# Kernel tuning notes

Measured on AMD Instinct MI355X. Metric: run time of the kernel, lower is better.

The kernel has to match this reference:

```python
import jax, jax.numpy as jnp
import numpy as np

FEATURE_DIM = 512


def setup_inputs() -> dict:
    key = jax.random.key(0)
    ks = jax.random.split(key, 12)
    B, Nv, Dv = 32, 1024, 768
    Nl, Dl = 77, 512
    D = FEATURE_DIM
    s = lambda fan_in: 1.0 / np.sqrt(fan_in)
    return {
        "fv": jax.random.normal(ks[0], (B, Nv, Dv), jnp.float32),
        "fl": jax.random.normal(ks[1], (B, Nl, Dl), jnp.float32),
        # linear_vk / linear_vv: Dv -> D (stored as [in, out])
        "W_vk": jax.random.uniform(ks[2], (Dv, D), jnp.float32, -s(Dv), s(Dv)),
        "b_vk": jax.random.uniform(ks[3], (D,), jnp.float32, -s(Dv), s(Dv)),
        "W_vv": jax.random.uniform(ks[4], (Dv, D), jnp.float32, -s(Dv), s(Dv)),
        "b_vv": jax.random.uniform(ks[5], (D,), jnp.float32, -s(Dv), s(Dv)),
        # linear_lk / linear_lv: Dl -> D
        "W_lk": jax.random.uniform(ks[6], (Dl, D), jnp.float32, -s(Dl), s(Dl)),
        "b_lk": jax.random.uniform(ks[7], (D,), jnp.float32, -s(Dl), s(Dl)),
        "W_lv": jax.random.uniform(ks[8], (Dl, D), jnp.float32, -s(Dl), s(Dl)),
        "b_lv": jax.random.uniform(ks[9], (D,), jnp.float32, -s(Dl), s(Dl)),
        # linear_m: nl(77) -> 768
        "W_m": jax.random.uniform(ks[10], (Nl, 768), jnp.float32, -s(Nl), s(Nl)),
        "b_m": jax.random.uniform(ks[11], (768,), jnp.float32, -s(Nl), s(Nl)),
    }


def reference(fv, fl, W_vk, b_vk, W_vv, b_vv, W_lk, b_lk, W_lv, b_lv, W_m, b_m):
    # projections
    fk_v = jnp.einsum("bvd,de->bve", fv, W_vk) + b_vk   # [B, Nv, D]
    fv_v = jnp.einsum("bvd,de->bve", fv, W_vv) + b_vv   # [B, Nv, D]
    fk_l = jnp.einsum("bld,de->ble", fl, W_lk) + b_lk   # [B, Nl, D]
    fv_l = jnp.einsum("bld,de->ble", fl, W_lv) + b_lv   # [B, Nl, D]
    # shared score matrix [B, Nl, Nv]
    a_raw = jnp.einsum("ble,bve->blv", fk_l, fk_v) / jnp.sqrt(
        jnp.asarray(FEATURE_DIM, fk_l.dtype))
    # dual softmax: over Nv for language queries, over Nl for vision queries
    fa_v = jnp.einsum("blv,bve->ble", jax.nn.softmax(a_raw, axis=-1), fv_v)  # [B, Nl, D]
    fa_l = jnp.einsum("bvl,ble->bve",
                      jax.nn.softmax(jnp.swapaxes(a_raw, -1, -2), axis=-1),
                      fv_l)                                                  # [B, Nv, D]
    # fm = fa_v @ fa_l^T -> [B, Nl, Nv]; transpose(1,2) -> [B, Nv, Nl]
    fm = jnp.einsum("bve,ble->bvl", fa_l, fa_v)          # [B, Nv, Nl]
    return jnp.einsum("bvl,lo->bvo", fm, W_m) + b_m      # [B, Nv, 768]
```

## Files before the change

### kernel.cpp

```cpp
#include <hip/hip_runtime.h>


using s16x8  = __attribute__((ext_vector_type(8))) short;
using f32x4v = __attribute__((ext_vector_type(4))) float;

__device__ __forceinline__ unsigned short f2bf(float f) {
  unsigned int u = __float_as_uint(f);
  u += 0x7fffu + ((u >> 16) & 1u);
  return (unsigned short)(u >> 16);
}
__device__ __forceinline__ float bf2f(unsigned short h) {
  return __uint_as_float(((unsigned int)h) << 16);
}
__device__ __forceinline__ void split2(float v, unsigned short &hh, unsigned short &ll) {
  hh = f2bf(v);
  ll = f2bf(v - bf2f(hh));
}
__device__ __forceinline__ void split8v(float4 a, float4 b, s16x8& H, s16x8& L) {
  unsigned short hh, ll;
  split2(a.x, hh, ll); H[0] = (short)hh; L[0] = (short)ll;
  split2(a.y, hh, ll); H[1] = (short)hh; L[1] = (short)ll;
  split2(a.z, hh, ll); H[2] = (short)hh; L[2] = (short)ll;
  split2(a.w, hh, ll); H[3] = (short)hh; L[3] = (short)ll;
  split2(b.x, hh, ll); H[4] = (short)hh; L[4] = (short)ll;
  split2(b.y, hh, ll); H[5] = (short)hh; L[5] = (short)ll;
  split2(b.z, hh, ll); H[6] = (short)hh; L[6] = (short)ll;
  split2(b.w, hh, ll); H[7] = (short)hh; L[7] = (short)ll;
}

__device__ __forceinline__ void gload16(const unsigned short* g, unsigned short* l) {
  __builtin_amdgcn_global_load_lds(
      (const __attribute__((address_space(1))) unsigned int*)(const void*)g,
      (__attribute__((address_space(3))) unsigned int*)(void*)l,
      16, 0, 0);
}

__global__ __launch_bounds__(256) void prep_weight(const float* __restrict__ W,
                                                   unsigned short* __restrict__ Wh,
                                                   unsigned short* __restrict__ Wl,
                                                   int K, int N, int Kpad) {
  __shared__ float tile[32][33];
  int nb = blockIdx.x * 32, kb = blockIdx.y * 32;
  int tx = threadIdx.x & 31, ty = threadIdx.x >> 5;
  #pragma unroll
  for (int i = 0; i < 32; i += 8) {
    int k = kb + ty + i, n = nb + tx;
    tile[ty + i][tx] = (k < K && n < N) ? W[(long)k * N + n] : 0.f;
  }
  __syncthreads();
  #pragma unroll
  for (int i = 0; i < 32; i += 8) {
    int n = nb + ty + i, k = kb + tx;
    if (n < N && k < Kpad) {
      unsigned short hh, ll;
      split2(tile[tx][ty + i], hh, ll);
      Wh[(long)n * Kpad + k] = hh;
      Wl[(long)n * Kpad + k] = ll;
    }
  }
}

struct GemmArgs {
  const unsigned short *Ah, *Alo, *Bh, *Blo;
  const float *Af;
  int K;
  int Mld, Nld;
  int lda, ldb;
  long long sA, sB;
};

template <bool AF32, bool SWZ, class Epi>
__global__ __launch_bounds__(256, 2) void gemm2(GemmArgs g, Epi epi) {
  __shared__ __align__(16) unsigned short sm[32768];

  int bidx = blockIdx.x, bidy = blockIdx.y;
  if constexpr (SWZ) {
    int nx = gridDim.x;
    int nwg = nx * gridDim.y;
    int orig = bidx + bidy * nx;
    int swz = (orig & 7) * (nwg >> 3) + (orig >> 3);
    bidx = swz % nx; bidy = swz / nx;
  }

  const int t    = threadIdx.x;
  const int b    = blockIdx.z;
  const int m0   = bidy * 128;
  const int n0   = bidx * 128;
  const int lane = t & 63;
  const int w    = t >> 6;
  const int wr   = (w >> 1) * 64;
  const int wc   = (w & 1) * 64;

  const long long aBase = (long long)b * g.sA;
  const long long bBase = (long long)b * g.sB;

  const int rw  = (w << 5) + (lane >> 2);
  const int cl  = lane & 3;
  const int sck = ((cl ^ ((rw >> 1) & 3)) << 3);
  int br0 = n0 + rw;      if (br0 > g.Nld - 1) br0 = g.Nld - 1;
  int br1 = n0 + rw + 16; if (br1 > g.Nld - 1) br1 = g.Nld - 1;
  const long long bR0d = bBase + (long long)br0 * g.ldb + sck;
  const long long bR1d = bBase + (long long)br1 * g.ldb + sck;
  int ar0 = m0 + rw;      if (ar0 > g.Mld - 1) ar0 = g.Mld - 1;
  int ar1 = m0 + rw + 16; if (ar1 > g.Mld - 1) ar1 = g.Mld - 1;
  const long long aR0d = aBase + (long long)ar0 * g.lda + sck;
  const long long aR1d = aBase + (long long)ar1 * g.lda + sck;
  const int dQ0 = w * 1024;
  const int dQ1 = w * 1024 + 512;

  const int rA0 = t >> 2, rA1 = 64 + (t >> 2), cc = t & 3;
  const int cOff = cc << 3;
  int mr0 = m0 + rA0; if (mr0 > g.Mld - 1) mr0 = g.Mld - 1;
  int mr1 = m0 + rA1; if (mr1 > g.Mld - 1) mr1 = g.Mld - 1;
  const long long aR0 = aBase + (long long)mr0 * g.lda;
  const long long aR1 = aBase + (long long)mr1 * g.lda;
  const int wA0 = rA0 * 32 + ((cc ^ ((rA0 >> 1) & 3)) << 3);
  const int wA1 = rA1 * 32 + ((cc ^ ((rA1 >> 1) & 3)) << 3);

  int roffA[4], roffB[4];
  #pragma unroll
  for (int i = 0; i < 4; ++i) {
    int row = wr + i * 16 + (lane & 15);
    int ch  = lane >> 4;
    roffA[i] = row * 32 + ((ch ^ ((row >> 1) & 3)) << 3);
    row = wc + i * 16 + (lane & 15);
    roffB[i] = row * 32 + ((ch ^ ((row >> 1) & 3)) << 3);
  }

  f32x4v acc[4][4];
  #pragma unroll
  for (int i = 0; i < 4; ++i)
    #pragma unroll
    for (int j = 0; j < 4; ++j)
      #pragma unroll
      for (int r = 0; r < 4; ++r) acc[i][j][r] = 0.f;

  float4 pa0, pa1, pa2, pa3;

  auto issueDMA = [&](int k0, int p) {
    unsigned short* bb = sm + p * 16384;
    gload16(g.Bh  + (bR0d + k0), bb + 8192  + dQ0);
    gload16(g.Bh  + (bR1d + k0), bb + 8192  + dQ1);
    gload16(g.Blo + (bR0d + k0), bb + 12288 + dQ0);
    gload16(g.Blo + (bR1d + k0), bb + 12288 + dQ1);
    if constexpr (!AF32) {
      gload16(g.Ah  + (aR0d + k0), bb + dQ0);
      gload16(g.Ah  + (aR1d + k0), bb + dQ1);
      gload16(g.Alo + (aR0d + k0), bb + 4096 + dQ0);
      gload16(g.Alo + (aR1d + k0), bb + 4096 + dQ1);
    }
  };
  auto issueLoadsA = [&](int k0) {
    if constexpr (AF32) {
      const float* s0 = g.Af + (aR0 + k0 + cOff);
      const float* s1 = g.Af + (aR1 + k0 + cOff);
      pa0 = *(const float4*)s0; pa1 = *(const float4*)(s0 + 4);
      pa2 = *(const float4*)s1; pa3 = *(const float4*)(s1 + 4);
    }
  };
  auto writeStageA = [&](int p) {
    if constexpr (AF32) {
      unsigned short* base = sm + p * 16384;
      s16x8 H, L;
      split8v(pa0, pa1, H, L);
      *(s16x8*)(base + wA0) = H; *(s16x8*)(base + 4096 + wA0) = L;
      split8v(pa2, pa3, H, L);
      *(s16x8*)(base + wA1) = H; *(s16x8*)(base + 4096 + wA1) = L;
    }
  };

  issueDMA(0, 0);
  issueLoadsA(0);
  writeStageA(0);
  int p = 0;
  const int nkt = g.K >> 5;
  for (int kt = 0; kt < nkt; ++kt) {
    asm volatile("s_waitcnt vmcnt(0)" ::: "memory");
    __syncthreads();
    if (kt + 1 < nkt) {
      issueDMA((kt + 1) << 5, p ^ 1);
      issueLoadsA((kt + 1) << 5);
    }
    unsigned short* base = sm + p * 16384;
    s16x8 ah[4], al[4], bh[4], bl[4];
    #pragma unroll
    for (int i = 0; i < 4; ++i) {
      ah[i] = *(const s16x8*)(base + roffA[i]);
      al[i] = *(const s16x8*)(base + 4096 + roffA[i]);
    }
    #pragma unroll
    for (int j = 0; j < 4; ++j) {
      bh[j] = *(const s16x8*)(base + 8192  + roffB[j]);
      bl[j] = *(const s16x8*)(base + 12288 + roffB[j]);
    }
    #pragma unroll
    for (int i = 0; i < 4; ++i)
      #pragma unroll
      for (int j = 0; j < 4; ++j) {
        acc[i][j] = __builtin_amdgcn_mfma_f32_16x16x32_bf16(ah[i], bh[j], acc[i][j], 0, 0, 0);
        acc[i][j] = __builtin_amdgcn_mfma_f32_16x16x32_bf16(ah[i], bl[j], acc[i][j], 0, 0, 0);
        acc[i][j] = __builtin_amdgcn_mfma_f32_16x16x32_bf16(al[i], bh[j], acc[i][j], 0, 0, 0);
      }
    if (kt + 1 < nkt) writeStageA(p ^ 1);
    p ^= 1;
  }
  #pragma unroll
  for (int i = 0; i < 4; ++i)
    #pragma unroll
    for (int j = 0; j < 4; ++j) {
      int mm = m0 + wr + i * 16 + ((lane >> 4) << 2);
      int nn = n0 + wc + j * 16 + (lane & 15);
      epi(b, mm, nn, acc[i][j]);
    }
}

struct EpiBF16Pair {
  unsigned short *h, *lo; const float* bias; long long bs; int ld; int Mst;
  __device__ void operator()(int b, int m, int n, f32x4v v) const {
    float bb = bias ? bias[n] : 0.f;
    #pragma unroll
    for (int r = 0; r < 4; ++r) {
      int mm = m + r;
      if (mm < Mst) {
        long long o = (long long)b * bs + (long long)mm * ld + n;
        unsigned short hh, ll;
        split2(v[r] + bb, hh, ll);
        h[o] = hh; lo[o] = ll;
      }
    }
  }
};

struct EpiDualL {
  unsigned short *kh, *kl, *vh, *vl; const float *bk, *bv;
  __device__ void operator()(int, int m, int n, f32x4v v) const {
    bool lo512 = n < 512;
    float bb = lo512 ? bk[n] : bv[n - 512];
    int nn = lo512 ? n : n - 512;
    unsigned short* H = lo512 ? kh : vh;
    unsigned short* L = lo512 ? kl : vl;
    #pragma unroll
    for (int r = 0; r < 4; ++r) {
      int mm = m + r;
      if (mm < 2464) {
        long long o = (long long)mm * 512 + nn;
        unsigned short hh, ll;
        split2(v[r] + bb, hh, ll);
        H[o] = hh; L[o] = ll;
      }
    }
  }
};

struct EpiDualV {
  unsigned short *kh, *kl, *vh, *vl; const float *bk, *bv;
  __device__ void operator()(int, int m, int n, f32x4v v) const {
    if (n < 512) {
      float bb = bk[n];
      #pragma unroll
      for (int r = 0; r < 4; ++r) {
        long long o = (long long)(m + r) * 512 + n;
        unsigned short hh, ll;
        split2(v[r] + bb, hh, ll);
        kh[o] = hh; kl[o] = ll;
      }
    } else {
      int b2 = m >> 10, vv = m & 1023;
      float bb = bv[n - 512];
      ushort4 H, L;
      split2(v[0] + bb, H.x, L.x); split2(v[1] + bb, H.y, L.y);
      split2(v[2] + bb, H.z, L.z); split2(v[3] + bb, H.w, L.w);
      long long o = ((long long)b2 * 512 + (n - 512)) * 1024 + vv;
      *(ushort4*)(vh + o) = H;
      *(ushort4*)(vl + o) = L;
    }
  }
};

struct EpiScore {
  float* out;
  __device__ void operator()(int b, int m, int n, f32x4v v) const {
    #pragma unroll
    for (int r = 0; r < 4; ++r) {
      int mm = m + r;
      if (mm < 77)
        out[((long long)b * 77 + mm) * 1024 + n] = v[r] * 0.04419417382415922f;
    }
  }
};

struct EpiTransT {
  unsigned short *h, *lo;
  __device__ void operator()(int b, int m, int n, f32x4v v) const {
    #pragma unroll
    for (int r = 0; r < 4; ++r) {
      int mm = m + r;
      float val = (mm < 77) ? v[r] : 0.f;
      long long o = (long long)b * 98304 + (long long)n * 128 + mm;
      unsigned short hh, ll;
      split2(val, hh, ll);
      h[o] = hh; lo[o] = ll;
    }
  }
};

struct EpiOutB {
  float* out; const float* bias;
  __device__ void operator()(int b, int m, int n, f32x4v v) const {
    float bb = bias[n];
    #pragma unroll
    for (int r = 0; r < 4; ++r)
      out[(long long)(b * 1024 + m + r) * 768 + n] = v[r] + bb;
  }
};

__global__ __launch_bounds__(256) void softmax_rows(const float* __restrict__ a,
                                                    unsigned short* __restrict__ Ph,
                                                    unsigned short* __restrict__ Plo) {
  long row = blockIdx.x;
  const float* src = a + row * 1024;
  int t = threadIdx.x;
  float4 x = ((const float4*)src)[t];
  float mx = fmaxf(fmaxf(x.x, x.y), fmaxf(x.z, x.w));
  #pragma unroll
  for (int o = 32; o; o >>= 1) mx = fmaxf(mx, __shfl_xor(mx, o));
  __shared__ float red[4], red2[4];
  int w = t >> 6;
  if ((t & 63) == 0) red[w] = mx;
  __syncthreads();
  mx = fmaxf(fmaxf(red[0], red[1]), fmaxf(red[2], red[3]));
  float e0 = __expf(x.x - mx), e1 = __expf(x.y - mx);
  float e2 = __expf(x.z - mx), e3 = __expf(x.w - mx);
  float s = e0 + e1 + e2 + e3;
  #pragma unroll
  for (int o = 32; o; o >>= 1) s += __shfl_xor(s, o);
  if ((t & 63) == 0) red2[w] = s;
  __syncthreads();
  s = red2[0] + red2[1] + red2[2] + red2[3];
  float inv = 1.f / s;
  ushort4 H, L;
  split2(e0 * inv, H.x, L.x); split2(e1 * inv, H.y, L.y);
  split2(e2 * inv, H.z, L.z); split2(e3 * inv, H.w, L.w);
  long o = row * 1024 + (long)t * 4;
  *(ushort4*)(Ph + o)  = H;
  *(ushort4*)(Plo + o) = L;
}

__global__ __launch_bounds__(128) void softmax_cols(const float* __restrict__ a,
                                                    unsigned short* __restrict__ Ph,
                                                    unsigned short* __restrict__ Plo) {
  __shared__ float tile[77 * 129];
  __shared__ float inv[128];
  int t = threadIdx.x;
  int c = blockIdx.x;
  int b = blockIdx.y;
  const float* src = a + (long)b * 77 * 1024 + c * 128;
  for (int r = 0; r < 77; ++r) tile[r * 129 + t] = src[(long)r * 1024 + t];
  __syncthreads();
  float mx = -1e30f;
  for (int r = 0; r < 77; ++r) mx = fmaxf(mx, tile[r * 129 + t]);
  float s = 0.f;
  for (int r = 0; r < 77; ++r) {
    float e = __expf(tile[r * 129 + t] - mx);
    tile[r * 129 + t] = e;
    s += e;
  }
  inv[t] = 1.f / s;
  __syncthreads();
  unsigned short* dh = Ph  + ((long)b * 1024 + c * 128) * 128;
  unsigned short* dl = Plo + ((long)b * 1024 + c * 128) * 128;
  for (int vb = 0; vb < 128; vb += 2) {
    int v = vb + (t >> 6);
    int k = (t & 63) * 2;
    float iv = inv[v];
    float p0 = (k     < 77) ? tile[k * 129 + v] * iv       : 0.f;
    float p1 = (k + 1 < 77) ? tile[(k + 1) * 129 + v] * iv : 0.f;
    ushort2 H, L;
    split2(p0, H.x, L.x); split2(p1, H.y, L.y);
    *(ushort2*)(dh + (long)v * 128 + k) = H;
    *(ushort2*)(dl + (long)v * 128 + k) = L;
  }
}

extern "C" void kernel_launch(void* const* d_in, const int* in_sizes, int n_in,
                              void* d_out, int out_size, void* d_ws, size_t ws_size,
                              hipStream_t stream) {
  const float* fv   = (const float*)d_in[0];
  const float* fl   = (const float*)d_in[1];
  const float* W_vk = (const float*)d_in[2];
  const float* b_vk = (const float*)d_in[3];
  const float* W_vv = (const float*)d_in[4];
  const float* b_vv = (const float*)d_in[5];
  const float* W_lk = (const float*)d_in[6];
  const float* b_lk = (const float*)d_in[7];
  const float* W_lv = (const float*)d_in[8];
  const float* b_lv = (const float*)d_in[9];
  const float* W_m  = (const float*)d_in[10];
  const float* b_m  = (const float*)d_in[11];

  char* base = (char*)d_ws;
  size_t off = 0;
  auto take = [&](size_t bytes) -> char* {
    char* p = base + off;
    off = (off + bytes + 255) & ~(size_t)255;
    return p;
  };

  unsigned short* wcatv_h = (unsigned short*)take(1572864);
  unsigned short* wcatv_l = (unsigned short*)take(1572864);
  unsigned short* wcatl_h = (unsigned short*)take(1048576);
  unsigned short* wcatl_l = (unsigned short*)take(1048576);
  unsigned short* wm_h    = (unsigned short*)take(196608);
  unsigned short* wm_l    = (unsigned short*)take(196608);
  unsigned short* fkl_h  = (unsigned short*)take(2523136);
  unsigned short* fkl_l  = (unsigned short*)take(2523136);
  unsigned short* fvl_h  = (unsigned short*)take(2523136);
  unsigned short* fvl_l  = (unsigned short*)take(2523136);
  unsigned short* fkv_h  = (unsigned short*)take(33554432);
  unsigned short* fkv_l  = (unsigned short*)take(33554432);
  unsigned short* fvvT_h = (unsigned short*)take(33554432);
  unsigned short* fvvT_l = (unsigned short*)take(33554432);
  float*          araw   = (float*)take(10092544);
  unsigned short* p1_h   = (unsigned short*)take(5046272);
  unsigned short* p1_l   = (unsigned short*)take(5046272);
  unsigned short* p2t_h  = (unsigned short*)take(8388608);
  unsigned short* p2t_l  = (unsigned short*)take(8388608);
  unsigned short* fav_h  = (unsigned short*)take(4194304);
  unsigned short* fav_l  = (unsigned short*)take(4194304);
  unsigned short* s_h    = (unsigned short*)take(1048576);
  unsigned short* s_l    = (unsigned short*)take(1048576);
  unsigned short* tt_h   = (unsigned short*)take(6291456);
  unsigned short* tt_l   = (unsigned short*)take(6291456);

  if (off > ws_size) return;

  prep_weight<<<dim3(16, 24), 256, 0, stream>>>(W_vk, wcatv_h, wcatv_l, 768, 512, 768);
  prep_weight<<<dim3(16, 24), 256, 0, stream>>>(W_vv, wcatv_h + 512 * 768, wcatv_l + 512 * 768, 768, 512, 768);
  prep_weight<<<dim3(16, 16), 256, 0, stream>>>(W_lk, wcatl_h, wcatl_l, 512, 512, 512);
  prep_weight<<<dim3(16, 16), 256, 0, stream>>>(W_lv, wcatl_h + 512 * 512, wcatl_l + 512 * 512, 512, 512, 512);
  prep_weight<<<dim3(24, 4), 256, 0, stream>>>(W_m, wm_h, wm_l, 77, 768, 128);

  {
    GemmArgs g{}; g.Af = fl; g.Bh = wcatl_h; g.Blo = wcatl_l;
    g.K = 512; g.Mld = 2464; g.Nld = 1024; g.lda = 512; g.ldb = 512; g.sA = 0; g.sB = 0;
    EpiDualL e{fkl_h, fkl_l, fvl_h, fvl_l, b_lk, b_lv};
    gemm2<true, false, EpiDualL><<<dim3(8, 20, 1), 256, 0, stream>>>(g, e);
  }
  {
    GemmArgs g{}; g.Af = fv; g.Bh = wcatv_h; g.Blo = wcatv_l;
    g.K = 768; g.Mld = 32768; g.Nld = 1024; g.lda = 768; g.ldb = 768; g.sA = 0; g.sB = 0;
    EpiDualV e{fkv_h, fkv_l, fvvT_h, fvvT_l, b_vk, b_vv};
    gemm2<true, true, EpiDualV><<<dim3(8, 256, 1), 256, 0, stream>>>(g, e);
  }
  {
    GemmArgs g{}; g.Ah = fkl_h; g.Alo = fkl_l; g.Bh = fkv_h; g.Blo = fkv_l;
    g.K = 512; g.Mld = 77; g.Nld = 1024; g.lda = 512; g.ldb = 512;
    g.sA = 77 * 512; g.sB = 1024 * 512;
    EpiScore e{araw};
    gemm2<false, false, EpiScore><<<dim3(8, 1, 32), 256, 0, stream>>>(g, e);
  }
  softmax_rows<<<2464, 256, 0, stream>>>(araw, p1_h, p1_l);
  softmax_cols<<<dim3(8, 32), 128, 0, stream>>>(araw, p2t_h, p2t_l);
  {
    GemmArgs g{}; g.Ah = p1_h; g.Alo = p1_l; g.Bh = fvvT_h; g.Blo = fvvT_l;
    g.K = 1024; g.Mld = 77; g.Nld = 512; g.lda = 1024; g.ldb = 1024;
    g.sA = 77 * 1024; g.sB = 512 * 1024;
    EpiBF16Pair e{fav_h, fav_l, nullptr, 128 * 512, 512, 128};
    gemm2<false, false, EpiBF16Pair><<<dim3(4, 1, 32), 256, 0, stream>>>(g, e);
  }
  {
    GemmArgs g{}; g.Ah = fvl_h; g.Alo = fvl_l; g.Bh = fav_h; g.Blo = fav_l;
    g.K = 512; g.Mld = 77; g.Nld = 128; g.lda = 512; g.ldb = 512;
    g.sA = 77 * 512; g.sB = 128 * 512;
    EpiBF16Pair e{s_h, s_l, nullptr, 128 * 128, 128, 128};
    gemm2<false, false, EpiBF16Pair><<<dim3(1, 1, 32), 256, 0, stream>>>(g, e);
  }
  {
    GemmArgs g{}; g.Ah = s_h; g.Alo = s_l; g.Bh = wm_h; g.Blo = wm_l;
    g.K = 128; g.Mld = 128; g.Nld = 768; g.lda = 128; g.ldb = 128;
    g.sA = 128 * 128; g.sB = 0;
    EpiTransT e{tt_h, tt_l};
    gemm2<false, false, EpiTransT><<<dim3(6, 1, 32), 256, 0, stream>>>(g, e);
  }
  {
    GemmArgs g{}; g.Ah = p2t_h; g.Alo = p2t_l; g.Bh = tt_h; g.Blo = tt_l;
    g.K = 128; g.Mld = 1024; g.Nld = 768; g.lda = 128; g.ldb = 128;
    g.sA = 1024 * 128; g.sB = 768 * 128;
    EpiOutB e{(float*)d_out, b_m};
    gemm2<false, false, EpiOutB><<<dim3(6, 8, 32), 256, 0, stream>>>(g, e);
  }
  (void)in_sizes; (void)n_in; (void)out_size;
}
```

Measured before the change: 585.7 us.

## Single-buffer GEMM LDS, raise occupancy, and add narrow-N tiles for small GEMMs

The GEMM kernel drops its LDS double buffer for a single stage with an extra barrier per k-step, and raises launch bounds from 2 to 4 blocks per CU. It is also templated on the N-tile width, so the small batched GEMMs use 64-wide N tiles and launch twice as many blocks. The aim is more resident waves to hide latency and better CU fill for the tiny per-batch GEMMs. The cost is that global loads are no longer overlapped with MFMA compute within a block, and the tighter register budget may cause spills.

```diff
diff --git a/kernel.cpp b/kernel.cpp
--- a/kernel.cpp
+++ b/kernel.cpp
@@ -69,9 +69,16 @@
   long long sA, sB;
 };
 
-template <bool AF32, bool SWZ, class Epi>
-__global__ __launch_bounds__(256, 2) void gemm2(GemmArgs g, Epi epi) {
-  __shared__ __align__(16) unsigned short sm[32768];
+template <bool AF32, bool SWZ, int NJ, class Epi>
+__global__ __launch_bounds__(256, 4) void gemm3(GemmArgs g, Epi epi) {
+  constexpr int BN  = NJ * 32;
+  constexpr int ASZ = 128 * 32;
+  constexpr int BSZ = BN * 32;
+  __shared__ __align__(16) unsigned short sm[2 * ASZ + 2 * BSZ];
+  unsigned short* sAh = sm;
+  unsigned short* sAl = sm + ASZ;
+  unsigned short* sBh = sm + 2 * ASZ;
+  unsigned short* sBl = sm + 2 * ASZ + BSZ;
 
   int bidx = blockIdx.x, bidy = blockIdx.y;
   if constexpr (SWZ) {
@@ -85,28 +92,31 @@
   const int t    = threadIdx.x;
   const int b    = blockIdx.z;
   const int m0   = bidy * 128;
-  const int n0   = bidx * 128;
+  const int n0   = bidx * BN;
   const int lane = t & 63;
   const int w    = t >> 6;
   const int wr   = (w >> 1) * 64;
-  const int wc   = (w & 1) * 64;
+  const int wc   = (w & 1) * (NJ * 16);
 
   const long long aBase = (long long)b * g.sA;
   const long long bBase = (long long)b * g.sB;
 
-  const int rw  = (w << 5) + (lane >> 2);
-  const int cl  = lane & 3;
-  const int sck = ((cl ^ ((rw >> 1) & 3)) << 3);
-  int br0 = n0 + rw;      if (br0 > g.Nld - 1) br0 = g.Nld - 1;
-  int br1 = n0 + rw + 16; if (br1 > g.Nld - 1) br1 = g.Nld - 1;
-  const long long bR0d = bBase + (long long)br0 * g.ldb + sck;
-  const long long bR1d = bBase + (long long)br1 * g.ldb + sck;
-  int ar0 = m0 + rw;      if (ar0 > g.Mld - 1) ar0 = g.Mld - 1;
-  int ar1 = m0 + rw + 16; if (ar1 > g.Mld - 1) ar1 = g.Mld - 1;
-  const long long aR0d = aBase + (long long)ar0 * g.lda + sck;
-  const long long aR1d = aBase + (long long)ar1 * g.lda + sck;
-  const int dQ0 = w * 1024;
-  const int dQ1 = w * 1024 + 512;
+  const int clk = lane & 3;
+  const int rwB = (NJ == 4) ? ((w << 5) + (lane >> 2)) : ((w << 4) + (lane >> 2));
+  const int sckB = ((clk ^ ((rwB >> 1) & 3)) << 3);
+  int br0 = n0 + rwB;      if (br0 > g.Nld - 1) br0 = g.Nld - 1;
+  int br1 = n0 + rwB + 16; if (br1 > g.Nld - 1) br1 = g.Nld - 1;
+  const long long bR0d = bBase + (long long)br0 * g.ldb + sckB;
+  const long long bR1d = bBase + (long long)br1 * g.ldb + sckB;
+  const int dB0 = (NJ == 4) ? (w << 10) : (w << 9);
+  const int dB1 = dB0 + 512;
+  const int rwA = (w << 5) + (lane >> 2);
+  const int sckA = ((clk ^ ((rwA >> 1) & 3)) << 3);
+  int arD0 = m0 + rwA;      if (arD0 > g.Mld - 1) arD0 = g.Mld - 1;
+  int arD1 = m0 + rwA + 16; if (arD1 > g.Mld - 1) arD1 = g.Mld - 1;
+  const long long aR0d = aBase + (long long)arD0 * g.lda + sckA;
+  const long long aR1d = aBase + (long long)arD1 * g.lda + sckA;
+  const int dA0 = w << 10, dA1 = (w << 10) + 512;
 
   const int rA0 = t >> 2, rA1 = 64 + (t >> 2), cc = t & 3;
   const int cOff = cc << 3;
@@ -117,40 +127,45 @@
   const int wA0 = rA0 * 32 + ((cc ^ ((rA0 >> 1) & 3)) << 3);
   const int wA1 = rA1 * 32 + ((cc ^ ((rA1 >> 1) & 3)) << 3);
 
-  int roffA[4], roffB[4];
+  int roffA[4], roffB[NJ];
   #pragma unroll
   for (int i = 0; i < 4; ++i) {
     int row = wr + i * 16 + (lane & 15);
     int ch  = lane >> 4;
     roffA[i] = row * 32 + ((ch ^ ((row >> 1) & 3)) << 3);
-    row = wc + i * 16 + (lane & 15);
-    roffB[i] = row * 32 + ((ch ^ ((row >> 1) & 3)) << 3);
-  }
-
-  f32x4v acc[4][4];
+  }
+  #pragma unroll
+  for (int j = 0; j < NJ; ++j) {
+    int row = wc + j * 16 + (lane & 15);
+    int ch  = lane >> 4;
+    roffB[j] = row * 32 + ((ch ^ ((row >> 1) & 3)) << 3);
+  }
+
+  f32x4v acc[4][NJ];
   #pragma unroll
   for (int i = 0; i < 4; ++i)
     #pragma unroll
-    for (int j = 0; j < 4; ++j)
+    for (int j = 0; j < NJ; ++j)
       #pragma unroll
       for (int r = 0; r < 4; ++r) acc[i][j][r] = 0.f;
 
   float4 pa0, pa1, pa2, pa3;
 
-  auto issueDMA = [&](int k0, int p) {
-    unsigned short* bb = sm + p * 16384;
-    gload16(g.Bh  + (bR0d + k0), bb + 8192  + dQ0);
-    gload16(g.Bh  + (bR1d + k0), bb + 8192  + dQ1);
-    gload16(g.Blo + (bR0d + k0), bb + 12288 + dQ0);
-    gload16(g.Blo + (bR1d + k0), bb + 12288 + dQ1);
+  auto issueDMA = [&](int k0) {
+    gload16(g.Bh  + (bR0d + k0), sBh + dB0);
+    gload16(g.Blo + (bR0d + k0), sBl + dB0);
+    if constexpr (NJ == 4) {
+      gload16(g.Bh  + (bR1d + k0), sBh + dB1);
+      gload16(g.Blo + (bR1d + k0), sBl + dB1);
+    }
     if constexpr (!AF32) {
-      gload16(g.Ah  + (aR0d + k0), bb + dQ0);
-      gload16(g.Ah  + (aR1d + k0), bb + dQ1);
-      gload16(g.Alo + (aR0d + k0), bb + 4096 + dQ0);
-      gload16(g.Alo + (aR1d + k0), bb + 4096 + dQ1);
+      gload16(g.Ah  + (aR0d + k0), sAh + dA0);
+      gload16(g.Ah  + (aR1d + k0), sAh + dA1);
+      gload16(g.Alo + (aR0d + k0), sAl + dA0);
+      gload16(g.Alo + (aR1d + k0), sAl + dA1);
     }
   };
-  auto issueLoadsA = [&](int k0) {
+  auto issueA = [&](int k0) {
     if constexpr (AF32) {
       const float* s0 = g.Af + (aR0 + k0 + cOff);
       const float* s1 = g.Af + (aR1 + k0 + cOff);
@@ -158,56 +173,52 @@
       pa2 = *(const float4*)s1; pa3 = *(const float4*)(s1 + 4);
     }
   };
-  auto writeStageA = [&](int p) {
+  auto writeA = [&]() {
     if constexpr (AF32) {
-      unsigned short* base = sm + p * 16384;
       s16x8 H, L;
       split8v(pa0, pa1, H, L);
-      *(s16x8*)(base + wA0) = H; *(s16x8*)(base + 4096 + wA0) = L;
+      *(s16x8*)(sAh + wA0) = H; *(s16x8*)(sAl + wA0) = L;
       split8v(pa2, pa3, H, L);
-      *(s16x8*)(base + wA1) = H; *(s16x8*)(base + 4096 + wA1) = L;
+      *(s16x8*)(sAh + wA1) = H; *(s16x8*)(sAl + wA1) = L;
     }
   };
 
-  issueDMA(0, 0);
-  issueLoadsA(0);
-  writeStageA(0);
-  int p = 0;
+  issueDMA(0);
+  if constexpr (AF32) { issueA(0); writeA(); }
   const int nkt = g.K >> 5;
   for (int kt = 0; kt < nkt; ++kt) {
     asm volatile("s_waitcnt vmcnt(0)" ::: "memory");
     __syncthreads();
-    if (kt + 1 < nkt) {
-      issueDMA((kt + 1) << 5, p ^ 1);
-      issueLoadsA((kt + 1) << 5);
-    }
-    unsigned short* base = sm + p * 16384;
-    s16x8 ah[4], al[4], bh[4], bl[4];
+    if (AF32 && kt + 1 < nkt) issueA((kt + 1) << 5);
+    s16x8 ah[4], al[4], bh[NJ], bl[NJ];
     #pragma unroll
     for (int i = 0; i < 4; ++i) {
-      ah[i] = *(const s16x8*)(base + roffA[i]);
-      al[i] = *(const s16x8*)(base + 4096 + roffA[i]);
-    }
-    #pragma unroll
-    for (int j = 0; j < 4; ++j) {
-      bh[j] = *(const s16x8*)(base + 8192  + roffB[j]);
-      bl[j] = *(const s16x8*)(base + 12288 + roffB[j]);
+      ah[i] = *(const s16x8*)(sAh + roffA[i]);
+      al[i] = *(const s16x8*)(sAl + roffA[i]);
+    }
+    #pragma unroll
+    for (int j = 0; j < NJ; ++j) {
+      bh[j] = *(const s16x8*)(sBh + roffB[j]);
+      bl[j] = *(const s16x8*)(sBl + roffB[j]);
     }
     #pragma unroll
     for (int i = 0; i < 4; ++i)
       #pragma unroll
-      for (int j = 0; j < 4; ++j) {
+      for (int j = 0; j < NJ; ++j) {
         acc[i][j] = __builtin_amdgcn_mfma_f32_16x16x32_bf16(ah[i], bh[j], acc[i][j], 0, 0, 0);
         acc[i][j] = __builtin_amdgcn_mfma_f32_16x16x32_bf16(ah[i], bl[j], acc[i][j], 0, 0, 0);
         acc[i][j] = __builtin_amdgcn_mfma_f32_16x16x32_bf16(al[i], bh[j], acc[i][j], 0, 0, 0);
       }
-    if (kt + 1 < nkt) writeStageA(p ^ 1);
-    p ^= 1;
+    __syncthreads();
+    if (kt + 1 < nkt) {
+      writeA();
+      issueDMA((kt + 1) << 5);
+    }
   }
   #pragma unroll
   for (int i = 0; i < 4; ++i)
     #pragma unroll
-    for (int j = 0; j < 4; ++j) {
+    for (int j = 0; j < NJ; ++j) {
       int mm = m0 + wr + i * 16 + ((lane >> 4) << 2);
       int nn = n0 + wc + j * 16 + (lane & 15);
       epi(b, mm, nn, acc[i][j]);
@@ -444,20 +455,20 @@
     GemmArgs g{}; g.Af = fl; g.Bh = wcatl_h; g.Blo = wcatl_l;
     g.K = 512; g.Mld = 2464; g.Nld = 1024; g.lda = 512; g.ldb = 512; g.sA = 0; g.sB = 0;
     EpiDualL e{fkl_h, fkl_l, fvl_h, fvl_l, b_lk, b_lv};
-    gemm2<true, false, EpiDualL><<<dim3(8, 20, 1), 256, 0, stream>>>(g, e);
+    gemm3<true, false, 4, EpiDualL><<<dim3(8, 20, 1), 256, 0, stream>>>(g, e);
   }
   {
     GemmArgs g{}; g.Af = fv; g.Bh = wcatv_h; g.Blo = wcatv_l;
     g.K = 768; g.Mld = 32768; g.Nld = 1024; g.lda = 768; g.ldb = 768; g.sA = 0; g.sB = 0;
     EpiDualV e{fkv_h, fkv_l, fvvT_h, fvvT_l, b_vk, b_vv};
-    gemm2<true, true, EpiDualV><<<dim3(8, 256, 1), 256, 0, stream>>>(g, e);
+    gemm3<true, true, 4, EpiDualV><<<dim3(8, 256, 1), 256, 0, stream>>>(g, e);
   }
   {
     GemmArgs g{}; g.Ah = fkl_h; g.Alo = fkl_l; g.Bh = fkv_h; g.Blo = fkv_l;
     g.K = 512; g.Mld = 77; g.Nld = 1024; g.lda = 512; g.ldb = 512;
     g.sA = 77 * 512; g.sB = 1024 * 512;
     EpiScore e{araw};
-    gemm2<false, false, EpiScore><<<dim3(8, 1, 32), 256, 0, stream>>>(g, e);
+    gemm3<false, false, 2, EpiScore><<<dim3(16, 1, 32), 256, 0, stream>>>(g, e);
   }
   softmax_rows<<<2464, 256, 0, stream>>>(araw, p1_h, p1_l);
   softmax_cols<<<dim3(8, 32), 128, 0, stream>>>(araw, p2t_h, p2t_l);
@@ -466,28 +477,28 @@
     g.K = 1024; g.Mld = 77; g.Nld = 512; g.lda = 1024; g.ldb = 1024;
     g.sA = 77 * 1024; g.sB = 512 * 1024;
     EpiBF16Pair e{fav_h, fav_l, nullptr, 128 * 512, 512, 128};
-    gemm2<false, false, EpiBF16Pair><<<dim3(4, 1, 32), 256, 0, stream>>>(g, e);
+    gemm3<false, false, 2, EpiBF16Pair><<<dim3(8, 1, 32), 256, 0, stream>>>(g, e);
   }
   {
     GemmArgs g{}; g.Ah = fvl_h; g.Alo = fvl_l; g.Bh = fav_h; g.Blo = fav_l;
     g.K = 512; g.Mld = 77; g.Nld = 128; g.lda = 512; g.ldb = 512;
     g.sA = 77 * 512; g.sB = 128 * 512;
     EpiBF16Pair e{s_h, s_l, nullptr, 128 * 128, 128, 128};
-    gemm2<false, false, EpiBF16Pair><<<dim3(1, 1, 32), 256, 0, stream>>>(g, e);
+    gemm3<false, false, 2, EpiBF16Pair><<<dim3(2, 1, 32), 256, 0, stream>>>(g, e);
   }
   {
     GemmArgs g{}; g.Ah = s_h; g.Alo = s_l; g.Bh = wm_h; g.Blo = wm_l;
     g.K = 128; g.Mld = 128; g.Nld = 768; g.lda = 128; g.ldb = 128;
     g.sA = 128 * 128; g.sB = 0;
     EpiTransT e{tt_h, tt_l};
-    gemm2<false, false, EpiTransT><<<dim3(6, 1, 32), 256, 0, stream>>>(g, e);
+    gemm3<false, false, 2, EpiTransT><<<dim3(12, 1, 32), 256, 0, stream>>>(g, e);
   }
   {
     GemmArgs g{}; g.Ah = p2t_h; g.Alo = p2t_l; g.Bh = tt_h; g.Blo = tt_l;
     g.K = 128; g.Mld = 1024; g.Nld = 768; g.lda = 128; g.ldb = 128;
     g.sA = 1024 * 128; g.sB = 768 * 128;
     EpiOutB e{(float*)d_out, b_m};
-    gemm2<false, false, EpiOutB><<<dim3(6, 8, 32), 256, 0, stream>>>(g, e);
+    gemm3<false, false, 4, EpiOutB><<<dim3(6, 8, 32), 256, 0, stream>>>(g, e);
   }
   (void)in_sizes; (void)n_in; (void)out_size;
 }
```

Result: slower. 650.3 us (+11.0%).
